# Kernel optimization log

Measured on AMD Instinct MI355X. Metric: run time of the kernel, lower is better.

Reference implementation:

```python
import jax, jax.numpy as jnp
import numpy as np

N = 50000      # nodes
F_IN = 500     # in_channels
MID = 64       # mid_layer_channel
H = 2          # heads
OUT = 40       # out_channels
E = 800000     # edges per order
ORDER = 3
NEG_SLOPE = 0.2


def _gat(x, edge_index, W, a_src, a_dst, b, concat):
    # PyG-style GATConv (eval mode, dropout off), with self loops.
    n = x.shape[0]
    heads, ch = a_src.shape
    h = (x @ W).reshape(n, heads, ch)                    # [N,H,C]
    loop = jnp.arange(n)
    src = jnp.concatenate([edge_index[0], loop])
    dst = jnp.concatenate([edge_index[1], loop])
    al_s = jnp.sum(h * a_src, axis=-1)                   # [N,H]
    al_d = jnp.sum(h * a_dst, axis=-1)                   # [N,H]
    e = jax.nn.leaky_relu(al_s[src] + al_d[dst], NEG_SLOPE)   # [Etot,H]
    m = jax.ops.segment_max(e, dst, num_segments=n)      # softmax over incoming edges per dst
    ex = jnp.exp(e - m[dst])
    den = jax.ops.segment_sum(ex, dst, num_segments=n)
    alpha = ex / (den[dst] + 1e-16)
    out = jax.ops.segment_sum(alpha[:, :, None] * h[src], dst, num_segments=n)  # [N,H,C]
    if concat:
        return out.reshape(n, heads * ch) + b
    return out.mean(axis=1) + b


def _aggr(states, Wmix, wfin):
    # NOrderAggrConv (depth=2): mix order states with [order,order] weights + ELU,
    # then reduce to a single state with a learned [order] combination.
    h = jnp.stack(states, axis=1)                        # [N,order,C]
    h = jax.nn.elu(jnp.einsum('nkc,kj->njc', h, Wmix))
    return jnp.einsum('nkc,k->nc', h, wfin)


def setup_inputs():
    key = jax.random.key(0)
    ks = jax.random.split(key, 40)
    d = {}
    d['node_feature'] = jax.random.normal(ks[0], (N, F_IN), jnp.float32)
    for o in range(ORDER):
        d[f'adj{o}'] = jax.random.randint(ks[1 + o], (2, E), 0, N)
    i = 4
    s = 0.05
    layer_dims = [(F_IN, MID, H * MID), (MID * H, OUT, OUT)]
    for l, (fin, c, bdim) in enumerate(layer_dims):
        for o in range(ORDER):
            d[f'W_{l}_{o}'] = jax.random.normal(ks[i], (fin, H * c), jnp.float32) * s; i += 1
            d[f'as_{l}_{o}'] = jax.random.normal(ks[i], (H, c), jnp.float32) * s; i += 1
            d[f'ad_{l}_{o}'] = jax.random.normal(ks[i], (H, c), jnp.float32) * s; i += 1
            d[f'b_{l}_{o}'] = jnp.zeros((bdim,), jnp.float32)
    for l in range(2):
        d[f'agg{l}_W'] = jax.random.normal(ks[i], (ORDER, ORDER), jnp.float32) * 0.5; i += 1
        d[f'agg{l}_w'] = jnp.full((ORDER,), 1.0 / ORDER, jnp.float32)
    return d


def reference(node_feature, adj0, adj1, adj2,
              W_0_0, as_0_0, ad_0_0, b_0_0,
              W_0_1, as_0_1, ad_0_1, b_0_1,
              W_0_2, as_0_2, ad_0_2, b_0_2,
              W_1_0, as_1_0, ad_1_0, b_1_0,
              W_1_1, as_1_1, ad_1_1, b_1_1,
              W_1_2, as_1_2, ad_1_2, b_1_2,
              agg0_W, agg0_w, agg1_W, agg1_w):
    adjs = (adj0, adj1, adj2)
    p0 = ((W_0_0, as_0_0, ad_0_0, b_0_0),
          (W_0_1, as_0_1, ad_0_1, b_0_1),
          (W_0_2, as_0_2, ad_0_2, b_0_2))
    p1 = ((W_1_0, as_1_0, ad_1_0, b_1_0),
          (W_1_1, as_1_1, ad_1_1, b_1_1),
          (W_1_2, as_1_2, ad_1_2, b_1_2))
    aggs = ((agg0_W, agg0_w), (agg1_W, agg1_w))
    x = node_feature  # eval mode: dropout is identity
    for l, params in enumerate((p0, p1)):
        concat = (l == 0)
        states = [jax.nn.elu(_gat(x, adjs[o], *params[o], concat)) for o in range(ORDER)]
        x = _aggr(states, *aggs[l])
    return jax.nn.log_softmax(x, axis=1)
```

## Files before the change

kernel.cpp:

```cpp
#include <hip/hip_runtime.h>
#include <cstdint>
#include <cstddef>
#include <math.h>


typedef __attribute__((ext_vector_type(8))) short short8;
typedef __attribute__((ext_vector_type(4))) float f32x4;
typedef __attribute__((ext_vector_type(2))) float f32x2;

struct P3f { const float* p[3]; };
struct P3c { const int* p[3]; };

__device__ __forceinline__ float leakyf(float x) { return x > 0.f ? x : 0.2f * x; }
__device__ __forceinline__ float eluf(float x)   { return x > 0.f ? x : expm1f(x); }

__device__ __forceinline__ unsigned short bf16r(float x) {
  unsigned int u = __float_as_uint(x);
  u += 0x7fffu + ((u >> 16) & 1u);
  return (unsigned short)(u >> 16);
}
__device__ __forceinline__ float bflo(unsigned int u) { return __uint_as_float(u << 16); }
__device__ __forceinline__ float bfhi(unsigned int u) { return __uint_as_float(u & 0xffff0000u); }

__device__ __forceinline__ void bf8_fma2(uint4 q, float xx, f32x2* a) {
  f32x2 v0 = {bflo(q.x), bfhi(q.x)};
  f32x2 v1 = {bflo(q.y), bfhi(q.y)};
  f32x2 v2 = {bflo(q.z), bfhi(q.z)};
  f32x2 v3 = {bflo(q.w), bfhi(q.w)};
  a[0] += xx * v0;
  a[1] += xx * v1;
  a[2] += xx * v2;
  a[3] += xx * v3;
}

__global__ __launch_bounds__(256) void zero_int_kernel(int* p, int n) {
  int i = blockIdx.x * blockDim.x + threadIdx.x;
  if (i < n) p[i] = 0;
}

__global__ __launch_bounds__(256) void convA_kernel(const float* __restrict__ A,
    unsigned short* __restrict__ Ab, int M, int K, int Kpad) {
  int i = blockIdx.x * blockDim.x + threadIdx.x;
  int row = i >> 6;
  int koff = (i & 63) * 8;
  if (row >= M) return;
  const float* ap = A + (size_t)row * K;
  unsigned short v[8];
  if (koff + 8 <= K) {
    float4 q0 = ((const float4*)(ap + koff))[0];
    float4 q1 = ((const float4*)(ap + koff))[1];
    v[0] = bf16r(q0.x); v[1] = bf16r(q0.y); v[2] = bf16r(q0.z); v[3] = bf16r(q0.w);
    v[4] = bf16r(q1.x); v[5] = bf16r(q1.y); v[6] = bf16r(q1.z); v[7] = bf16r(q1.w);
  } else {
#pragma unroll
    for (int k = 0; k < 8; ++k)
      v[k] = (koff + k < K) ? bf16r(ap[koff + k]) : (unsigned short)0;
  }
  *(uint4*)(Ab + (size_t)row * Kpad + koff) = *(const uint4*)v;
}

__global__ __launch_bounds__(256) void count3_kernel(P3c adj, int* __restrict__ cntb,
    int* __restrict__ posb, int E, int N) {
  int i = blockIdx.x * blockDim.x + threadIdx.x;
  int o = blockIdx.y;
  if (i < E) {
    int d = adj.p[o][E + i];
    posb[(size_t)o * E + i] = atomicAdd(&cntb[o * N + d], 1);
  }
}

#define SCAN_T 256
#define SCAN_VPT 8
#define SCAN_TILE 2048

__global__ __launch_bounds__(SCAN_T) void scan1_kernel(const int* __restrict__ cntb,
    int* __restrict__ rowptrb, int* __restrict__ bsums, int N) {
  __shared__ int lds[SCAN_T];
  const int o = blockIdx.y;
  const int* cnt = cntb + o * N;
  int* rowptr = rowptrb + o * (N + 1);
  int t = threadIdx.x;
  int base = blockIdx.x * SCAN_TILE + t * SCAN_VPT;
  int v[SCAN_VPT];
  int s = 0;
#pragma unroll
  for (int i = 0; i < SCAN_VPT; ++i) {
    int idx = base + i;
    int x = (idx < N) ? cnt[idx] : 0;
    s += x;
    v[i] = s;
  }
  lds[t] = s;
  __syncthreads();
  for (int off = 1; off < SCAN_T; off <<= 1) {
    int add = (t >= off) ? lds[t - off] : 0;
    __syncthreads();
    lds[t] += add;
    __syncthreads();
  }
  int excl = (t > 0) ? lds[t - 1] : 0;
#pragma unroll
  for (int i = 0; i < SCAN_VPT; ++i) {
    int idx = base + i;
    if (idx < N) rowptr[idx + 1] = excl + v[i];
  }
  if (t == SCAN_T - 1) bsums[o * 64 + blockIdx.x] = lds[t];
}

__global__ void scan2_kernel(int* bsums, int nb, int* rowptrb, int N) {
  if (threadIdx.x == 0 && blockIdx.x == 0) {
    for (int o = 0; o < 3; ++o) {
      int run = 0;
      for (int i = 0; i < nb; ++i) {
        int x = bsums[o * 64 + i];
        bsums[o * 64 + i] = run;
        run += x;
      }
      rowptrb[o * (N + 1)] = 0;
    }
  }
}

__global__ __launch_bounds__(256) void scan3_kernel(int* __restrict__ rowptrb,
    const int* __restrict__ bsums, int N) {
  int idx = blockIdx.x * blockDim.x + threadIdx.x;
  int o = blockIdx.y;
  if (idx < N) rowptrb[o * (N + 1) + idx + 1] += bsums[o * 64 + idx / SCAN_TILE];
}

__global__ __launch_bounds__(256) void fill3_kernel(P3c adj,
    const int* __restrict__ rowptrb, const int* __restrict__ posb,
    int* __restrict__ colvb, int E, int N) {
  int i = blockIdx.x * blockDim.x + threadIdx.x;
  int o = blockIdx.y;
  if (i < E) {
    const int* a = adj.p[o];
    int d = a[E + i];
    int pos = posb[(size_t)o * E + i];
    colvb[(size_t)o * E + rowptrb[o * (N + 1) + d] + pos] = a[i];
  }
}

__global__ __launch_bounds__(256) void alpha3_kernel(const int* __restrict__ rowptrB,
    const int* __restrict__ colvB, const float2* __restrict__ alsB,
    const float2* __restrict__ aldB, float2* __restrict__ alphB, int N, int E) {
  int w = blockIdx.x * blockDim.x + threadIdx.x;
  int o = blockIdx.y;
  if (w >= N) return;
  const int* rowptr = rowptrB + o * (N + 1);
  const int* colv = colvB + (size_t)o * E;
  const float2* als = alsB + (size_t)o * N;
  const float2 b = (aldB + (size_t)o * N)[w];
  float2* alph = alphB + (size_t)o * E;
  const int beg = rowptr[w], end = rowptr[w + 1];
  for (int j = beg; j < end; ++j) {
    int s = colv[j];
    float2 a = als[s];
    alph[j] = make_float2(__expf(leakyf(a.x + b.x)), __expf(leakyf(a.y + b.y)));
  }
}

__global__ __launch_bounds__(256) void conv_bt3_kernel(P3f W,
    unsigned short* __restrict__ BtB, int K, int NC, int Kpad) {
  int n = blockIdx.y;
  int o = blockIdx.z;
  int k = blockIdx.x * 256 + threadIdx.x;
  if (k >= Kpad) return;
  float v = (k < K) ? W.p[o][(size_t)k * NC + n] : 0.f;
  BtB[(size_t)o * NC * Kpad + (size_t)n * Kpad + k] = bf16r(v);
}

#define GBM 128
#define LDSTRIDE 40

template<int NT>
__global__ __launch_bounds__(256) void mfma_gemm_kernel(
    const unsigned short* __restrict__ Ab, const unsigned short* __restrict__ BtB,
    P3f asp, P3f adp, unsigned short* __restrict__ CbB,
    float2* __restrict__ alsB, float2* __restrict__ aldB, int M, int Kpad) {
  constexpr int NC = NT * 16;
  constexpr int CH = NT * 8;
  __shared__ unsigned short As[GBM * LDSTRIDE];
  __shared__ unsigned short Bs[NC * LDSTRIDE];
  const int t = threadIdx.x;
  const int o = blockIdx.y;
  const int wave = t >> 6, lane = t & 63;
  const int quad = lane >> 4, l16 = lane & 15;
  const int m0 = blockIdx.x * GBM;
  const unsigned short* Bt = BtB + (size_t)o * NC * Kpad;
  unsigned short* Cb = CbB + (size_t)o * M * NC;
  float2* al_s = alsB + (size_t)o * M;
  float2* al_d = aldB + (size_t)o * M;
  const float* a_src = asp.p[o];
  const float* a_dst = adp.p[o];

  f32x4 acc[2][NT];
#pragma unroll
  for (int i = 0; i < 2; ++i)
#pragma unroll
    for (int j = 0; j < NT; ++j) acc[i][j] = (f32x4){0.f, 0.f, 0.f, 0.f};

  const int arow = t >> 1;
  const int akoff = (t & 1) * 16;
  const int gm = m0 + arow;
  const unsigned short* arowp = Ab + (size_t)gm * Kpad;
  const unsigned short* browp = Bt + (size_t)arow * Kpad;

  for (int k0 = 0; k0 < Kpad; k0 += 32) {
    if (k0) __syncthreads();
    const int kb = k0 + akoff;
    {
      uint4 q0 = {0, 0, 0, 0}, q1 = {0, 0, 0, 0};
      if (gm < M) {
        const uint4* p = (const uint4*)(arowp + kb);
        q0 = p[0]; q1 = p[1];
      }
      short8* dst = (short8*)&As[arow * LDSTRIDE + akoff];
      union { uint4 q; short8 s; } c0, c1;
      c0.q = q0; c1.q = q1;
      dst[0] = c0.s;
      dst[1] = c1.s;
    }
    if (arow < NC) {
      const uint4* p = (const uint4*)(browp + kb);
      uint4 q0 = p[0], q1 = p[1];
      short8* dst = (short8*)&Bs[arow * LDSTRIDE + akoff];
      union { uint4 q; short8 s; } c0, c1;
      c0.q = q0; c1.q = q1;
      dst[0] = c0.s;
      dst[1] = c1.s;
    }
    __syncthreads();
    short8 af[2];
#pragma unroll
    for (int rt = 0; rt < 2; ++rt)
      af[rt] = *(const short8*)&As[(wave * 32 + rt * 16 + l16) * LDSTRIDE + quad * 8];
    short8 bfv[NT];
#pragma unroll
    for (int ct = 0; ct < NT; ++ct)
      bfv[ct] = *(const short8*)&Bs[(ct * 16 + l16) * LDSTRIDE + quad * 8];
#pragma unroll
    for (int rt = 0; rt < 2; ++rt)
#pragma unroll
      for (int ct = 0; ct < NT; ++ct)
        acc[rt][ct] = __builtin_amdgcn_mfma_f32_16x16x32_bf16(af[rt], bfv[ct],
                                                              acc[rt][ct], 0, 0, 0);
  }
  float asv[NT], adv[NT];
#pragma unroll
  for (int ct = 0; ct < NT; ++ct) {
    int col = ct * 16 + l16;
    asv[ct] = a_src[col];
    adv[ct] = a_dst[col];
  }
#pragma unroll
  for (int rt = 0; rt < 2; ++rt) {
    int gr0 = m0 + wave * 32 + rt * 16 + quad * 4;
#pragma unroll
    for (int r = 0; r < 4; ++r) {
      int gr = gr0 + r;
      float ps0 = 0.f, ps1 = 0.f, pd0 = 0.f, pd1 = 0.f;
#pragma unroll
      for (int ct = 0; ct < NT; ++ct) {
        int col = ct * 16 + l16;
        float v = acc[rt][ct][r];
        if (gr < M) Cb[(size_t)gr * NC + col] = bf16r(v);
        if (col < CH) { ps0 += v * asv[ct]; pd0 += v * adv[ct]; }
        else          { ps1 += v * asv[ct]; pd1 += v * adv[ct]; }
      }
#pragma unroll
      for (int off = 1; off < 16; off <<= 1) {
        ps0 += __shfl_xor(ps0, off, 64);
        ps1 += __shfl_xor(ps1, off, 64);
        pd0 += __shfl_xor(pd0, off, 64);
        pd1 += __shfl_xor(pd1, off, 64);
      }
      if (l16 == 0 && gr < M) {
        al_s[gr] = make_float2(ps0, ps1);
        al_d[gr] = make_float2(pd0, pd1);
      }
    }
  }
}

template<int C, int CONCAT>
__global__ __launch_bounds__(256) void gat_slot4_kernel(
    const unsigned short* __restrict__ hB, const float2* __restrict__ alsB,
    const float2* __restrict__ aldB, const int* __restrict__ rowptrB,
    const int* __restrict__ colvB, const float2* __restrict__ alphB,
    P3f biasp, unsigned short* __restrict__ outB, int N, int E) {
  constexpr int HC = 2 * C;
  constexpr int FLd = HC / 8;
  constexpr int HB = C / 8;
  constexpr int OW = CONCAT ? HC : C;
  const int o = blockIdx.y;
  const unsigned short* h = hB + (size_t)o * N * HC;
  const float2* al_s = alsB + (size_t)o * N;
  const float2* al_d = aldB + (size_t)o * N;
  const int* rowptr = rowptrB + o * (N + 1);
  const int* colv = colvB + (size_t)o * E;
  const float2* alph = alphB + (size_t)o * E;
  const float* bias = biasp.p[o];
  unsigned short* out = outB + (size_t)o * N * OW;

  const int gw = (blockIdx.x * blockDim.x + threadIdx.x) >> 6;
  const int lane = threadIdx.x & 63;
  const int slot = lane >> 4;
  const int f4 = lane & 15;
  const int w = gw * 4 + slot;
  if (gw * 4 >= N) return;
  const bool vn = w < N;
  const int wc = vn ? w : N - 1;
  const bool hl = f4 < FLd;

  const int beg = rowptr[wc];
  const int deg = vn ? (rowptr[wc + 1] - beg) : 0;
  int md = deg;
  md = max(md, __shfl_xor(md, 32, 64));
  md = max(md, __shfl_xor(md, 16, 64));

  const float2 ad = al_d[wc];
  const float2 asf = al_s[wc];
  const float xs0 = __expf(leakyf(asf.x + ad.x));
  const float xs1 = __expf(leakyf(asf.y + ad.y));
  float dp0 = xs0, dp1 = xs1;

  f32x2 acc[4] = {}, acc2[4] = {};
  if (hl) {
    uint4 q = ((const uint4*)(h + (size_t)wc * HC))[f4];
    bf8_fma2(q, (f4 < HB) ? xs0 : xs1, acc);
  }

  const float2 z2 = make_float2(0.f, 0.f);
  for (int t = 0; t < md; t += 4) {
    const int j0 = beg + t;
    const bool v0 = t < deg;
    const bool v1 = t + 1 < deg;
    const bool v2 = t + 2 < deg;
    const bool v3 = t + 3 < deg;
    const int s0 = v0 ? colv[j0] : 0;
    const int s1 = v1 ? colv[j0 + 1] : 0;
    const int s2 = v2 ? colv[j0 + 2] : 0;
    const int s3 = v3 ? colv[j0 + 3] : 0;
    const float2 a0 = v0 ? alph[j0] : z2;
    const float2 a1 = v1 ? alph[j0 + 1] : z2;
    const float2 a2 = v2 ? alph[j0 + 2] : z2;
    const float2 a3 = v3 ? alph[j0 + 3] : z2;
    uint4 q0 = make_uint4(0, 0, 0, 0), q1 = q0, q2 = q0, q3 = q0;
    if (v0 && hl) q0 = ((const uint4*)(h + (size_t)s0 * HC))[f4];
    if (v1 && hl) q1 = ((const uint4*)(h + (size_t)s1 * HC))[f4];
    if (v2 && hl) q2 = ((const uint4*)(h + (size_t)s2 * HC))[f4];
    if (v3 && hl) q3 = ((const uint4*)(h + (size_t)s3 * HC))[f4];
    dp0 += (a0.x + a1.x) + (a2.x + a3.x);
    dp1 += (a0.y + a1.y) + (a2.y + a3.y);
    if (v0 && hl) bf8_fma2(q0, (f4 < HB) ? a0.x : a0.y, acc);
    if (v1 && hl) bf8_fma2(q1, (f4 < HB) ? a1.x : a1.y, acc2);
    if (v2 && hl) bf8_fma2(q2, (f4 < HB) ? a2.x : a2.y, acc);
    if (v3 && hl) bf8_fma2(q3, (f4 < HB) ? a3.x : a3.y, acc2);
  }
#pragma unroll
  for (int i = 0; i < 4; ++i) acc[i] += acc2[i];

  const float inv0 = 1.f / (dp0 + 1e-16f), inv1 = 1.f / (dp1 + 1e-16f);
  if (CONCAT) {
    if (vn && hl) {
      const float xx = (f4 < HB) ? inv0 : inv1;
      const float* bp = bias + f4 * 8;
      unsigned int pk[4];
#pragma unroll
      for (int i = 0; i < 4; ++i) {
        unsigned short lo = bf16r(eluf(acc[i][0] * xx + bp[2 * i]));
        unsigned short hi = bf16r(eluf(acc[i][1] * xx + bp[2 * i + 1]));
        pk[i] = (unsigned int)lo | ((unsigned int)hi << 16);
      }
      ((uint4*)(out + (size_t)w * OW + f4 * 8))[0] = make_uint4(pk[0], pk[1], pk[2], pk[3]);
    }
  } else {
    float p[8];
#pragma unroll
    for (int i = 0; i < 4; ++i) {
      p[2 * i]     = __shfl(acc[i][0], lane + HB, 64);
      p[2 * i + 1] = __shfl(acc[i][1], lane + HB, 64);
    }
    if (vn && f4 < HB) {
      const float* bp = bias + f4 * 8;
      unsigned int pk[4];
#pragma unroll
      for (int i = 0; i < 4; ++i) {
        float v0 = 0.5f * (acc[i][0] * inv0 + p[2 * i] * inv1) + bp[2 * i];
        float v1 = 0.5f * (acc[i][1] * inv0 + p[2 * i + 1] * inv1) + bp[2 * i + 1];
        pk[i] = (unsigned int)bf16r(eluf(v0)) | ((unsigned int)bf16r(eluf(v1)) << 16);
      }
      ((uint4*)(out + (size_t)w * OW + f4 * 8))[0] = make_uint4(pk[0], pk[1], pk[2], pk[3]);
    }
  }
}

template<int BF16OUT>
__global__ __launch_bounds__(256) void mixb_kernel(const unsigned short* __restrict__ sb,
    const float* __restrict__ Wm, const float* __restrict__ wf,
    void* __restrict__ out, int perU) {
  int i = blockIdx.x * blockDim.x + threadIdx.x;
  if (i >= perU) return;
  const unsigned int* sp = (const unsigned int*)sb;
  unsigned int u0 = sp[i];
  unsigned int u1 = sp[perU + i];
  unsigned int u2 = sp[2 * perU + i];
  float a0 = bflo(u0), a1 = bfhi(u0);
  float b0 = bflo(u1), b1 = bfhi(u1);
  float c0 = bflo(u2), c1 = bfhi(u2);
  float r0 = 0.f, r1 = 0.f;
#pragma unroll
  for (int j = 0; j < 3; ++j) {
    float w0 = Wm[j], w1 = Wm[3 + j], w2 = Wm[6 + j], wj = wf[j];
    r0 += wj * eluf(a0 * w0 + b0 * w1 + c0 * w2);
    r1 += wj * eluf(a1 * w0 + b1 * w1 + c1 * w2);
  }
  if (BF16OUT) {
    ((unsigned int*)out)[i] = (unsigned int)bf16r(r0) | ((unsigned int)bf16r(r1) << 16);
  } else {
    ((float2*)out)[i] = make_float2(r0, r1);
  }
}

__global__ __launch_bounds__(256) void log_softmax_kernel(const float* __restrict__ x,
    float* __restrict__ out, int N, int C) {
  int w = (blockIdx.x * blockDim.x + threadIdx.x) >> 6;
  int lane = threadIdx.x & 63;
  if (w >= N) return;
  float v = (lane < C) ? x[(size_t)w * C + lane] : -INFINITY;
  float mx = v;
#pragma unroll
  for (int off = 1; off < 64; off <<= 1) mx = fmaxf(mx, __shfl_xor(mx, off, 64));
  float ex = (lane < C) ? expf(v - mx) : 0.f;
  float s = ex;
#pragma unroll
  for (int off = 1; off < 64; off <<= 1) s += __shfl_xor(s, off, 64);
  if (lane < C) out[(size_t)w * C + lane] = v - mx - logf(s);
}

extern "C" void kernel_launch(void* const* d_in, const int* in_sizes, int n_in,
                              void* d_out, int out_size, void* d_ws, size_t ws_size,
                              hipStream_t stream) {
  const int F_IN = 500;
  const int N = in_sizes[0] / F_IN;
  const int E = in_sizes[1] / 2;
  const int HC0 = 128;
  const int HC1 = 80;
  const int C1 = 40;
  const int K0pad = 512, K1pad = 128;

  const float* x0 = (const float*)d_in[0];
  P3c adj;
  adj.p[0] = (const int*)d_in[1];
  adj.p[1] = (const int*)d_in[2];
  adj.p[2] = (const int*)d_in[3];
  P3f W0p, as0p, ad0p, b0p, W1p, as1p, ad1p, b1p;
  for (int o = 0; o < 3; ++o) {
    W0p.p[o]  = (const float*)d_in[4 + 4 * o + 0];
    as0p.p[o] = (const float*)d_in[4 + 4 * o + 1];
    ad0p.p[o] = (const float*)d_in[4 + 4 * o + 2];
    b0p.p[o]  = (const float*)d_in[4 + 4 * o + 3];
    W1p.p[o]  = (const float*)d_in[16 + 4 * o + 0];
    as1p.p[o] = (const float*)d_in[16 + 4 * o + 1];
    ad1p.p[o] = (const float*)d_in[16 + 4 * o + 2];
    b1p.p[o]  = (const float*)d_in[16 + 4 * o + 3];
  }
  const float* agg0W = (const float*)d_in[28];
  const float* agg0w = (const float*)d_in[29];
  const float* agg1W = (const float*)d_in[30];
  const float* agg1w = (const float*)d_in[31];

  char* ws = (char*)d_ws;
  size_t off = 0;
  auto alloc = [&](size_t bytes) -> void* {
    off = (off + 255) & ~(size_t)255;
    void* p = ws + off;
    off += bytes;
    return p;
  };
  int* rowptrb = (int*)alloc((size_t)3 * (N + 1) * 4);
  int* colvb   = (int*)alloc((size_t)3 * E * 4);
  int* posb    = (int*)alloc((size_t)3 * E * 4);
  int* cntb    = (int*)alloc((size_t)3 * N * 4);
  int* bsums   = (int*)alloc(3 * 64 * 4);
  unsigned short* x0b = (unsigned short*)alloc((size_t)N * K0pad * 2);
  unsigned short* hB  = (unsigned short*)alloc((size_t)3 * N * HC0 * 2);
  unsigned short* stB = (unsigned short*)alloc((size_t)3 * N * HC0 * 2);
  float* x2 = (float*)alloc((size_t)N * C1 * 4);
  float2* alsB = (float2*)alloc((size_t)3 * N * 8);
  float2* aldB = (float2*)alloc((size_t)3 * N * 8);
  unsigned short* Bt0B = (unsigned short*)alloc((size_t)3 * HC0 * K0pad * 2);
  unsigned short* Bt1B = (unsigned short*)alloc((size_t)3 * HC1 * K1pad * 2);
  float2* alphb = (float2*)x0b;
  (void)ws_size;

  const int TB = 256;
  const int nbE = (E + TB - 1) / TB;
  const int nbN = (N + TB - 1) / TB;
  const int scanBlocks = (N + SCAN_TILE - 1) / SCAN_TILE;
  const int gemmBlocks = (N + GBM - 1) / GBM;
  const int slot4Blocks = (int)(((size_t)((N + 3) / 4) * 64 + TB - 1) / TB);
  const int lsBlocks = (int)(((size_t)N * 64 + TB - 1) / TB);

  convA_kernel<<<(int)(((size_t)N * 64 + TB - 1) / TB), TB, 0, stream>>>(
      x0, x0b, N, F_IN, K0pad);
  conv_bt3_kernel<<<dim3((K0pad + 255) / 256, HC0, 3), TB, 0, stream>>>(W0p, Bt0B, F_IN, HC0, K0pad);
  conv_bt3_kernel<<<dim3((K1pad + 255) / 256, HC1, 3), TB, 0, stream>>>(W1p, Bt1B, HC0, HC1, K1pad);

  zero_int_kernel<<<(3 * N + TB - 1) / TB, TB, 0, stream>>>(cntb, 3 * N);
  count3_kernel<<<dim3(nbE, 3), TB, 0, stream>>>(adj, cntb, posb, E, N);
  scan1_kernel<<<dim3(scanBlocks, 3), SCAN_T, 0, stream>>>(cntb, rowptrb, bsums, N);
  scan2_kernel<<<1, 64, 0, stream>>>(bsums, scanBlocks, rowptrb, N);
  scan3_kernel<<<dim3(nbN, 3), TB, 0, stream>>>(rowptrb, bsums, N);
  fill3_kernel<<<dim3(nbE, 3), TB, 0, stream>>>(adj, rowptrb, posb, colvb, E, N);

  mfma_gemm_kernel<8><<<dim3(gemmBlocks, 3), TB, 0, stream>>>(
      x0b, Bt0B, as0p, ad0p, hB, alsB, aldB, N, K0pad);
  alpha3_kernel<<<dim3(nbN, 3), TB, 0, stream>>>(rowptrb, colvb, alsB, aldB, alphb, N, E);
  gat_slot4_kernel<64, 1><<<dim3(slot4Blocks, 3), TB, 0, stream>>>(
      hB, alsB, aldB, rowptrb, colvb, alphb, b0p, stB, N, E);
  mixb_kernel<1><<<((N * HC0 / 2) + TB - 1) / TB, TB, 0, stream>>>(
      stB, agg0W, agg0w, stB, N * HC0 / 2);

  mfma_gemm_kernel<5><<<dim3(gemmBlocks, 3), TB, 0, stream>>>(
      stB, Bt1B, as1p, ad1p, hB, alsB, aldB, N, K1pad);
  alpha3_kernel<<<dim3(nbN, 3), TB, 0, stream>>>(rowptrb, colvb, alsB, aldB, alphb, N, E);
  gat_slot4_kernel<40, 0><<<dim3(slot4Blocks, 3), TB, 0, stream>>>(
      hB, alsB, aldB, rowptrb, colvb, alphb, b1p, stB, N, E);
  mixb_kernel<0><<<((N * C1 / 2) + TB - 1) / TB, TB, 0, stream>>>(
      stB, agg1W, agg1w, x2, N * C1 / 2);

  log_softmax_kernel<<<lsBlocks, TB, 0, stream>>>(x2, (float*)d_out, N, C1);
}
```

Measured before the change: 801.0 us.

## Split CSR count atomics into per-edge-segment counters to cut contention

The edge counting step now keeps separate per-node counters for each of 8 contiguous edge segments, so each segment's atomics land in a different address range. A new per-node scan turns the segment counters into offsets and produces total counts for the existing row-pointer scan. The fill step adds the segment offset to each edge's local position. posb and the segment counters reuse the hB and stB buffers. The cost is an extra kernel launch and an 8x larger counter array to zero and scan.

```diff
diff --git a/kernel.cpp b/kernel.cpp
--- a/kernel.cpp
+++ b/kernel.cpp
@@ -10,6 +10,9 @@
 
 struct P3f { const float* p[3]; };
 struct P3c { const int* p[3]; };
+
+#define SSEG 8
+#define SEGSH 17
 
 __device__ __forceinline__ float leakyf(float x) { return x > 0.f ? x : 0.2f * x; }
 __device__ __forceinline__ float eluf(float x)   { return x > 0.f ? x : expm1f(x); }
@@ -59,14 +62,32 @@
   *(uint4*)(Ab + (size_t)row * Kpad + koff) = *(const uint4*)v;
 }
 
-__global__ __launch_bounds__(256) void count3_kernel(P3c adj, int* __restrict__ cntb,
-    int* __restrict__ posb, int E, int N) {
+__global__ __launch_bounds__(256) void count3_kernel(P3c adj,
+    int* __restrict__ segcnt, int* __restrict__ posb, int E, int N) {
   int i = blockIdx.x * blockDim.x + threadIdx.x;
   int o = blockIdx.y;
   if (i < E) {
     int d = adj.p[o][E + i];
-    posb[(size_t)o * E + i] = atomicAdd(&cntb[o * N + d], 1);
-  }
+    int s = i >> SEGSH;
+    if (s > SSEG - 1) s = SSEG - 1;
+    posb[(size_t)o * E + i] = atomicAdd(&segcnt[((size_t)o * SSEG + s) * N + d], 1);
+  }
+}
+
+__global__ __launch_bounds__(256) void nodeseg_scan_kernel(int* __restrict__ segcnt,
+    int* __restrict__ cntb, int N) {
+  int n = blockIdx.x * blockDim.x + threadIdx.x;
+  int o = blockIdx.y;
+  if (n >= N) return;
+  int run = 0;
+#pragma unroll
+  for (int s = 0; s < SSEG; ++s) {
+    size_t idx = ((size_t)o * SSEG + s) * N + n;
+    int c = segcnt[idx];
+    segcnt[idx] = run;
+    run += c;
+  }
+  cntb[o * N + n] = run;
 }
 
 #define SCAN_T 256
@@ -129,14 +150,16 @@
 }
 
 __global__ __launch_bounds__(256) void fill3_kernel(P3c adj,
-    const int* __restrict__ rowptrb, const int* __restrict__ posb,
-    int* __restrict__ colvb, int E, int N) {
+    const int* __restrict__ rowptrb, const int* __restrict__ segcnt,
+    const int* __restrict__ posb, int* __restrict__ colvb, int E, int N) {
   int i = blockIdx.x * blockDim.x + threadIdx.x;
   int o = blockIdx.y;
   if (i < E) {
     const int* a = adj.p[o];
     int d = a[E + i];
-    int pos = posb[(size_t)o * E + i];
+    int s = i >> SEGSH;
+    if (s > SSEG - 1) s = SSEG - 1;
+    int pos = segcnt[((size_t)o * SSEG + s) * N + d] + posb[(size_t)o * E + i];
     colvb[(size_t)o * E + rowptrb[o * (N + 1) + d] + pos] = a[i];
   }
 }
@@ -481,7 +504,6 @@
   };
   int* rowptrb = (int*)alloc((size_t)3 * (N + 1) * 4);
   int* colvb   = (int*)alloc((size_t)3 * E * 4);
-  int* posb    = (int*)alloc((size_t)3 * E * 4);
   int* cntb    = (int*)alloc((size_t)3 * N * 4);
   int* bsums   = (int*)alloc(3 * 64 * 4);
   unsigned short* x0b = (unsigned short*)alloc((size_t)N * K0pad * 2);
@@ -493,6 +515,8 @@
   unsigned short* Bt0B = (unsigned short*)alloc((size_t)3 * HC0 * K0pad * 2);
   unsigned short* Bt1B = (unsigned short*)alloc((size_t)3 * HC1 * K1pad * 2);
   float2* alphb = (float2*)x0b;
+  int* posb   = (int*)hB;
+  int* segcnt = (int*)stB;
   (void)ws_size;
 
   const int TB = 256;
@@ -508,12 +532,13 @@
   conv_bt3_kernel<<<dim3((K0pad + 255) / 256, HC0, 3), TB, 0, stream>>>(W0p, Bt0B, F_IN, HC0, K0pad);
   conv_bt3_kernel<<<dim3((K1pad + 255) / 256, HC1, 3), TB, 0, stream>>>(W1p, Bt1B, HC0, HC1, K1pad);
 
-  zero_int_kernel<<<(3 * N + TB - 1) / TB, TB, 0, stream>>>(cntb, 3 * N);
-  count3_kernel<<<dim3(nbE, 3), TB, 0, stream>>>(adj, cntb, posb, E, N);
+  zero_int_kernel<<<(3 * SSEG * N + TB - 1) / TB, TB, 0, stream>>>(segcnt, 3 * SSEG * N);
+  count3_kernel<<<dim3(nbE, 3), TB, 0, stream>>>(adj, segcnt, posb, E, N);
+  nodeseg_scan_kernel<<<dim3(nbN, 3), TB, 0, stream>>>(segcnt, cntb, N);
   scan1_kernel<<<dim3(scanBlocks, 3), SCAN_T, 0, stream>>>(cntb, rowptrb, bsums, N);
   scan2_kernel<<<1, 64, 0, stream>>>(bsums, scanBlocks, rowptrb, N);
   scan3_kernel<<<dim3(nbN, 3), TB, 0, stream>>>(rowptrb, bsums, N);
-  fill3_kernel<<<dim3(nbE, 3), TB, 0, stream>>>(adj, rowptrb, posb, colvb, E, N);
+  fill3_kernel<<<dim3(nbE, 3), TB, 0, stream>>>(adj, rowptrb, segcnt, posb, colvb, E, N);
 
   mfma_gemm_kernel<8><<<dim3(gemmBlocks, 3), TB, 0, stream>>>(
       x0b, Bt0B, as0p, ad0p, hB, alsB, aldB, N, K0pad);
```

Result: no change. 816.4 us (+1.9%).

## Fuse edge-count atomics into layer-0 GEMM launch via interleaved block roles

Applied to the files above, without the earlier changes.

Merges the edge-degree counting kernel with the first-layer MFMA GEMM into one launch, with every ninth block doing GEMM work and the others doing atomic in-degree counting. The memory-bound atomic work can then overlap with the compute-bound GEMM, and one launch is removed. The GEMM now runs before the CSR scan and fill. The pos buffer reuses the stB workspace, which is not needed until later, to save allocation. Heterogeneous blocks can unbalance scheduling, and the shared-memory footprint of GEMM blocks also applies to the counting blocks.

```diff
diff --git a/kernel.cpp b/kernel.cpp
--- a/kernel.cpp
+++ b/kernel.cpp
@@ -174,19 +174,15 @@
 #define LDSTRIDE 40
 
 template<int NT>
-__global__ __launch_bounds__(256) void mfma_gemm_kernel(
+__device__ __forceinline__ void gemm_body(int m0, int o, int t,
     const unsigned short* __restrict__ Ab, const unsigned short* __restrict__ BtB,
     P3f asp, P3f adp, unsigned short* __restrict__ CbB,
-    float2* __restrict__ alsB, float2* __restrict__ aldB, int M, int Kpad) {
+    float2* __restrict__ alsB, float2* __restrict__ aldB, int M, int Kpad,
+    unsigned short* As, unsigned short* Bs) {
   constexpr int NC = NT * 16;
   constexpr int CH = NT * 8;
-  __shared__ unsigned short As[GBM * LDSTRIDE];
-  __shared__ unsigned short Bs[NC * LDSTRIDE];
-  const int t = threadIdx.x;
-  const int o = blockIdx.y;
   const int wave = t >> 6, lane = t & 63;
   const int quad = lane >> 4, l16 = lane & 15;
-  const int m0 = blockIdx.x * GBM;
   const unsigned short* Bt = BtB + (size_t)o * NC * Kpad;
   unsigned short* Cb = CbB + (size_t)o * M * NC;
   float2* al_s = alsB + (size_t)o * M;
@@ -279,6 +275,44 @@
         al_s[gr] = make_float2(ps0, ps1);
         al_d[gr] = make_float2(pd0, pd1);
       }
+    }
+  }
+}
+
+template<int NT>
+__global__ __launch_bounds__(256) void mfma_gemm_kernel(
+    const unsigned short* __restrict__ Ab, const unsigned short* __restrict__ BtB,
+    P3f asp, P3f adp, unsigned short* __restrict__ CbB,
+    float2* __restrict__ alsB, float2* __restrict__ aldB, int M, int Kpad) {
+  __shared__ unsigned short As[GBM * LDSTRIDE];
+  __shared__ unsigned short Bs[NT * 16 * LDSTRIDE];
+  gemm_body<NT>(blockIdx.x * GBM, blockIdx.y, threadIdx.x,
+                Ab, BtB, asp, adp, CbB, alsB, aldB, M, Kpad, As, Bs);
+}
+
+__global__ __launch_bounds__(256) void gemm0_count_kernel(
+    const unsigned short* __restrict__ Ab, const unsigned short* __restrict__ BtB,
+    P3f asp, P3f adp, unsigned short* __restrict__ CbB,
+    float2* __restrict__ alsB, float2* __restrict__ aldB, int M, int Kpad,
+    P3c adj, int* __restrict__ cntb, int* __restrict__ posb, int E, int N,
+    int nbG) {
+  __shared__ unsigned short As[GBM * LDSTRIDE];
+  __shared__ unsigned short Bs[128 * LDSTRIDE];
+  const int x = blockIdx.x;
+  const int o = blockIdx.y;
+  const int gx = x / 9;
+  const int rem = x - gx * 9;
+  if (rem == 0 && gx < nbG) {
+    gemm_body<8>(gx * GBM, o, threadIdx.x,
+                 Ab, BtB, asp, adp, CbB, alsB, aldB, M, Kpad, As, Bs);
+  } else {
+    int nG = (x + 8) / 9;
+    if (nG > nbG) nG = nbG;
+    const int c = x - nG;
+    const int i = c * 256 + threadIdx.x;
+    if (i < E) {
+      int d = adj.p[o][E + i];
+      posb[(size_t)o * E + i] = atomicAdd(&cntb[o * N + d], 1);
     }
   }
 }
@@ -481,7 +515,6 @@
   };
   int* rowptrb = (int*)alloc((size_t)3 * (N + 1) * 4);
   int* colvb   = (int*)alloc((size_t)3 * E * 4);
-  int* posb    = (int*)alloc((size_t)3 * E * 4);
   int* cntb    = (int*)alloc((size_t)3 * N * 4);
   int* bsums   = (int*)alloc(3 * 64 * 4);
   unsigned short* x0b = (unsigned short*)alloc((size_t)N * K0pad * 2);
@@ -493,6 +526,7 @@
   unsigned short* Bt0B = (unsigned short*)alloc((size_t)3 * HC0 * K0pad * 2);
   unsigned short* Bt1B = (unsigned short*)alloc((size_t)3 * HC1 * K1pad * 2);
   float2* alphb = (float2*)x0b;
+  int* posb = (int*)stB;
   (void)ws_size;
 
   const int TB = 256;
@@ -509,14 +543,21 @@
   conv_bt3_kernel<<<dim3((K1pad + 255) / 256, HC1, 3), TB, 0, stream>>>(W1p, Bt1B, HC0, HC1, K1pad);
 
   zero_int_kernel<<<(3 * N + TB - 1) / TB, TB, 0, stream>>>(cntb, 3 * N);
-  count3_kernel<<<dim3(nbE, 3), TB, 0, stream>>>(adj, cntb, posb, E, N);
+  if (8 * gemmBlocks >= nbE) {
+    gemm0_count_kernel<<<dim3(gemmBlocks * 9, 3), TB, 0, stream>>>(
+        x0b, Bt0B, as0p, ad0p, hB, alsB, aldB, N, K0pad,
+        adj, cntb, posb, E, N, gemmBlocks);
+  } else {
+    count3_kernel<<<dim3(nbE, 3), TB, 0, stream>>>(adj, cntb, posb, E, N);
+    mfma_gemm_kernel<8><<<dim3(gemmBlocks, 3), TB, 0, stream>>>(
+        x0b, Bt0B, as0p, ad0p, hB, alsB, aldB, N, K0pad);
+  }
+
   scan1_kernel<<<dim3(scanBlocks, 3), SCAN_T, 0, stream>>>(cntb, rowptrb, bsums, N);
   scan2_kernel<<<1, 64, 0, stream>>>(bsums, scanBlocks, rowptrb, N);
   scan3_kernel<<<dim3(nbN, 3), TB, 0, stream>>>(rowptrb, bsums, N);
   fill3_kernel<<<dim3(nbE, 3), TB, 0, stream>>>(adj, rowptrb, posb, colvb, E, N);
 
-  mfma_gemm_kernel<8><<<dim3(gemmBlocks, 3), TB, 0, stream>>>(
-      x0b, Bt0B, as0p, ad0p, hB, alsB, aldB, N, K0pad);
   alpha3_kernel<<<dim3(nbN, 3), TB, 0, stream>>>(rowptrb, colvb, alsB, aldB, alphb, N, E);
   gat_slot4_kernel<64, 1><<<dim3(slot4Blocks, 3), TB, 0, stream>>>(
       hB, alsB, aldB, rowptrb, colvb, alphb, b0p, stB, N, E);
```

Result: faster. 760.3 us (-5.1%).
